# Kernel tuning notes

Measured on AMD Instinct MI355X. Metric: run time of the kernel, lower is better.

## Reference

```python
import jax, jax.numpy as jnp
import numpy as np

NS = 50000   # sentence (src) nodes, unit==1
NW = 50000   # word (dst) nodes, unit==0
E = 1600000  # sw edges
IN_DIM = 128
OUT_DIM = 64


def setup_inputs() -> dict:
    key = jax.random.key(0)
    k1, k2, k3, k4, k5, k6 = jax.random.split(key, 6)
    return {
        "h": jax.random.normal(k1, (NS, IN_DIM), dtype=jnp.float32),
        "W_fc": jax.random.normal(k2, (IN_DIM, OUT_DIM), dtype=jnp.float32) * 0.05,
        "w_attn": jax.random.normal(k3, (2 * OUT_DIM, 1), dtype=jnp.float32) * 0.05,
        "weight": jax.random.uniform(k4, (E,), dtype=jnp.float32),
        "src_idx": jax.random.randint(k5, (E,), 0, NS, dtype=jnp.int32),
        "dst_idx": jax.random.randint(k6, (E,), 0, NW, dtype=jnp.int32),
    }


def reference(h, W_fc, w_attn, weight, src_idx, dst_idx):
    # z = fc(h) on source (sentence) nodes only; dst (word) nodes have z == 0 in DGL
    z = h @ W_fc                                   # [NS, OUT_DIM]
    zs = z[src_idx]                                # [E, OUT_DIM] gather src features
    # attn_fc(cat(z_src, z_dst)) with z_dst == 0 -> only first half of w_attn acts
    wa_src = w_attn[:OUT_DIM, 0]                   # [OUT_DIM]
    e = jax.nn.leaky_relu(zs @ wa_src)             # [E], slope 0.01 (torch default)
    e = weight * e                                 # tfidf edge weight scaling
    # edge-softmax per destination node (segment softmax over ragged mailbox)
    m = jax.ops.segment_max(e, dst_idx, num_segments=NW)          # [NW]
    m = jnp.where(jnp.isfinite(m), m, 0.0)                        # empty nodes
    ex = jnp.exp(e - m[dst_idx])                                  # [E]
    den = jax.ops.segment_sum(ex, dst_idx, num_segments=NW)       # [NW]
    alpha = ex / jnp.where(den == 0.0, 1.0, den)[dst_idx]         # [E]
    # weighted scatter-sum of neighbor features into dst nodes
    out = jax.ops.segment_sum(alpha[:, None] * zs, dst_idx, num_segments=NW)
    return out                                     # [NW, OUT_DIM]
```

## Files before the change

kernel.cpp:

```cpp
#include <hip/hip_runtime.h>
#include <hip/hip_fp16.h>
#include <math.h>

#define NS_ 50000
#define NW_ 50000
#define IN_DIM_ 128
#define OUT_DIM_ 64

#define NSLAB 512
#define NB 1563
#define CAPS 1280
#define CAPP 2304

__device__ inline float leaky01(float x) { return x > 0.0f ? x : 0.01f * x; }

__global__ __launch_bounds__(256) void fc_kernel(const float* __restrict__ h,
                                                 const float* __restrict__ Wfc,
                                                 const float* __restrict__ w_attn,
                                                 __half* __restrict__ z16,
                                                 float* __restrict__ t) {
    __shared__ float hs[64 * IN_DIM_];
    int tid = threadIdx.x;
    int lane = tid & 63;
    int wv = tid >> 6;

    float Wc[IN_DIM_];
#pragma unroll
    for (int k = 0; k < IN_DIM_; ++k) Wc[k] = Wfc[k * OUT_DIM_ + lane];
    float wa = w_attn[lane];

    int row0 = blockIdx.x * 64;
    int nrows = NS_ - row0; if (nrows > 64) nrows = 64;

    const float4* hg = (const float4*)(h + (size_t)row0 * IN_DIM_);
    float4* hs4 = (float4*)hs;
    int nv = nrows * (IN_DIM_ / 4);
    for (int i = tid; i < nv; i += 256) hs4[i] = hg[i];
    __syncthreads();

    int rend = wv * 16 + 16; if (rend > nrows) rend = nrows;
    for (int r = wv * 16; r < rend; r += 2) {
        bool two = (r + 1 < rend);
        const float4* h0 = (const float4*)(hs + r * IN_DIM_);
        const float4* h1 = (const float4*)(hs + (two ? r + 1 : r) * IN_DIM_);
        float a0 = 0, a1 = 0, a2 = 0, a3 = 0;
        float b0 = 0, b1 = 0, b2 = 0, b3 = 0;
#pragma unroll
        for (int k4 = 0; k4 < IN_DIM_ / 4; ++k4) {
            float4 u = h0[k4];
            float4 v = h1[k4];
            a0 = fmaf(u.x, Wc[4 * k4 + 0], a0);
            a1 = fmaf(u.y, Wc[4 * k4 + 1], a1);
            a2 = fmaf(u.z, Wc[4 * k4 + 2], a2);
            a3 = fmaf(u.w, Wc[4 * k4 + 3], a3);
            b0 = fmaf(v.x, Wc[4 * k4 + 0], b0);
            b1 = fmaf(v.y, Wc[4 * k4 + 1], b1);
            b2 = fmaf(v.z, Wc[4 * k4 + 2], b2);
            b3 = fmaf(v.w, Wc[4 * k4 + 3], b3);
        }
        float za = (a0 + a1) + (a2 + a3);
        float zb = (b0 + b1) + (b2 + b3);
        z16[(size_t)(row0 + r) * OUT_DIM_ + lane] = __float2half(za);
        if (two) z16[(size_t)(row0 + r + 1) * OUT_DIM_ + lane] = __float2half(zb);
        float ta = za * wa, tb = zb * wa;
#pragma unroll
        for (int off = 32; off > 0; off >>= 1) {
            ta += __shfl_down(ta, off, 64);
            tb += __shfl_down(tb, off, 64);
        }
        if (lane == 0) {
            t[row0 + r] = ta;
            if (two) t[row0 + r + 1] = tb;
        }
    }
}

__global__ __launch_bounds__(1024) void partition_kernel(const float* __restrict__ weight,
                                                         const int* __restrict__ src,
                                                         const int* __restrict__ dst,
                                                         const float* __restrict__ t,
                                                         unsigned* __restrict__ meta_sb,
                                                         int2* __restrict__ edata,
                                                         int E, int slab_e) {
    __shared__ int hist[NB];
    __shared__ int cur[NB];
    __shared__ int wsum[16];
    int tid = threadIdx.x;
    int lane = tid & 63;
    int wv = tid >> 6;
    int s = blockIdx.x;
    int e0 = s * slab_e;
    int e1 = e0 + slab_e; if (e1 > E) e1 = E;
    int cnt = e1 - e0;

    for (int i = tid; i < NB; i += 1024) hist[i] = 0;
    __syncthreads();

    float exr0 = 0, exr1 = 0, exr2 = 0, exr3 = 0;
    int mr0 = 0, mr1 = 0, mr2 = 0, mr3 = 0;
#define PART_LOAD(P, EXR, MR)                                              \
    {                                                                      \
        int i = tid + (P) * 1024;                                          \
        if (i < cnt) {                                                     \
            int e = e0 + i;                                                \
            int sr = src[e];                                               \
            int d = dst[e];                                                \
            float ev = weight[e] * leaky01(t[sr]);                         \
            EXR = __expf(ev);                                              \
            MR = sr | ((d & 31) << 16) | ((d >> 5) << 21);                 \
            atomicAdd(&hist[d >> 5], 1);                                   \
        }                                                                  \
    }
    PART_LOAD(0, exr0, mr0)
    PART_LOAD(1, exr1, mr1)
    PART_LOAD(2, exr2, mr2)
    PART_LOAD(3, exr3, mr3)
#undef PART_LOAD
    __syncthreads();

    int i0 = 2 * tid, i1 = 2 * tid + 1;
    int h0 = (i0 < NB) ? hist[i0] : 0;
    int h1 = (i1 < NB) ? hist[i1] : 0;
    int pairv = h0 + h1;
    int incl = pairv;
#pragma unroll
    for (int off = 1; off < 64; off <<= 1) {
        int u = __shfl_up(incl, off, 64);
        if (lane >= off) incl += u;
    }
    if (lane == 63) wsum[wv] = incl;
    __syncthreads();
    int woff = 0;
    for (int w = 0; w < wv; ++w) woff += wsum[w];
    incl += woff;
    int base = incl - pairv;
    if (i0 < NB) {
        cur[i0] = base;
        meta_sb[(size_t)s * NB + i0] = ((unsigned)h0 << 16) | (unsigned)base;
    }
    if (i1 < NB) {
        int b1 = base + h0;
        cur[i1] = b1;
        meta_sb[(size_t)s * NB + i1] = ((unsigned)h1 << 16) | (unsigned)b1;
    }
    __syncthreads();

#define PART_STORE(P, EXR, MR)                                             \
    {                                                                      \
        int i = tid + (P) * 1024;                                          \
        if (i < cnt) {                                                     \
            int b = ((unsigned)MR) >> 21;                                  \
            int pos = atomicAdd(&cur[b], 1);                               \
            edata[e0 + pos] = make_int2(__float_as_int(EXR), MR & 0x1FFFFF); \
        }                                                                  \
    }
    PART_STORE(0, exr0, mr0)
    PART_STORE(1, exr1, mr1)
    PART_STORE(2, exr2, mr2)
    PART_STORE(3, exr3, mr3)
#undef PART_STORE
}

__global__ __launch_bounds__(256) void meta_transpose_kernel(const unsigned* __restrict__ meta,
                                                             unsigned* __restrict__ metaT) {
    __shared__ unsigned tile[64][65];
    int b0 = blockIdx.x * 64;
    int s0 = blockIdx.y * 64;
    int tx = threadIdx.x & 63, ty = threadIdx.x >> 6;
    for (int r = ty; r < 64; r += 4) {
        int b = b0 + tx;
        tile[r][tx] = (b < NB) ? meta[(size_t)(s0 + r) * NB + b] : 0u;
    }
    __syncthreads();
    for (int r = ty; r < 64; r += 4) {
        int b = b0 + r;
        if (b < NB) metaT[(size_t)b * NSLAB + s0 + tx] = tile[tx][r];
    }
}

__global__ __launch_bounds__(512) void aggregate_kernel(const unsigned* __restrict__ metaT,
                                                        const int2* __restrict__ edata,
                                                        const __half* __restrict__ z16,
                                                        float* __restrict__ out,
                                                        int slab_e) {
    __shared__ int2 sbuf[CAPS];
    __shared__ int2 sorted[CAPP];
    __shared__ unsigned short soff[NSLAB];
    __shared__ int arr[NSLAB + 1];
    __shared__ int wsum[8];
    __shared__ float dden[32];
    __shared__ int dcnt[32];
    __shared__ int dbase[33];

    int orig = blockIdx.x;
    {
        const int nwg = NB, nx = 8;
        int q = nwg / nx, r = nwg % nx;
        int xcd = orig % nx, idx = orig / nx;
        orig = (xcd < r) ? xcd * (q + 1) + idx : r * (q + 1) + (xcd - r) * q + idx;
    }
    int b = orig;
    int tid = threadIdx.x;
    int lane = tid & 63;
    int wv = tid >> 6;

    int cntv;
    {
        unsigned mv = metaT[(size_t)b * NSLAB + tid];
        soff[tid] = (unsigned short)(mv & 0xFFFFu);
        cntv = (int)(mv >> 16);
    }
    if (tid < 32) { dden[tid] = 0.0f; dcnt[tid] = 0; }
    for (int i = tid; i < CAPP; i += 512) sorted[i] = make_int2(0, 0);

    int incl = cntv;
#pragma unroll
    for (int off = 1; off < 64; off <<= 1) {
        int u = __shfl_up(incl, off, 64);
        if (lane >= off) incl += u;
    }
    if (lane == 63) wsum[wv] = incl;
    __syncthreads();
    int woff = 0;
    for (int w = 0; w < wv; ++w) woff += wsum[w];
    incl += woff;
    arr[tid + 1] = incl;
    if (tid == 0) arr[0] = 0;
    __syncthreads();

    int total = arr[NSLAB];
    if (total > CAPS) total = CAPS;

    int gid = tid >> 1, l2 = tid & 1;
    for (int s = gid; s < NSLAB; s += 256) {
        int base = arr[s];
        int len = arr[s + 1] - base;
        int so = (int)soff[s];
        for (int j = l2; j < len; j += 2) {
            int p = base + j;
            if (p < CAPS) {
                int2 e = edata[(size_t)s * slab_e + so + j];
                sbuf[p] = e;
                int d5 = (e.y >> 16) & 31;
                atomicAdd(&dcnt[d5], 1);
                atomicAdd(&dden[d5], __int_as_float(e.x));
            }
        }
    }
    __syncthreads();

    if (tid < 32) {
        int v = dcnt[tid];
        int pv = (v + 31) & ~31;
        int iv = pv;
#pragma unroll
        for (int off = 1; off < 32; off <<= 1) {
            int u = __shfl_up(iv, off, 64);
            if (tid >= off) iv += u;
        }
        dbase[tid + 1] = iv;
        dcnt[tid] = iv - pv;
        if (tid == 0) dbase[0] = 0;
    }
    __syncthreads();

    for (int k = tid; k < total; k += 512) {
        int2 e = sbuf[k];
        int d5 = (e.y >> 16) & 31;
        int pos = atomicAdd(&dcnt[d5], 1);
        if (pos < CAPP) sorted[pos] = e;
    }
    __syncthreads();

    int qg = lane >> 4;
    int dl = lane & 15;
    const unsigned short* z16u = (const unsigned short*)z16;
    for (int q = 0; q < 4; ++q) {
        int d5 = wv * 4 + q;
        int d = b * 32 + d5;
        if (d >= NW_) continue;
        int a0 = dbase[d5];
        int npad = dbase[d5 + 1] - a0;
        float dn = dden[d5];
        float invdn = (dn > 0.0f) ? 1.0f / dn : 0.0f;
        float c0 = 0.f, c1 = 0.f, c2 = 0.f, c3 = 0.f;
        for (int j = 0; j < npad; j += 32) {
            int2 ee[8];
#pragma unroll
            for (int u = 0; u < 8; ++u) ee[u] = sorted[a0 + j + u * 4 + qg];
            uint2 zz[8];
#pragma unroll
            for (int u = 0; u < 8; ++u) {
                int srcr = ee[u].y & 0xFFFF;
                zz[u] = *(const uint2*)(z16u + (size_t)srcr * 64 + dl * 4);
            }
#pragma unroll
            for (int u = 0; u < 8; ++u) {
                float ex = __int_as_float(ee[u].x);
                __half2 p0 = *(__half2*)&zz[u].x;
                __half2 p1 = *(__half2*)&zz[u].y;
                c0 = fmaf(ex, __low2float(p0), c0);
                c1 = fmaf(ex, __high2float(p0), c1);
                c2 = fmaf(ex, __low2float(p1), c2);
                c3 = fmaf(ex, __high2float(p1), c3);
            }
        }
        c0 += __shfl_xor(c0, 16, 64); c1 += __shfl_xor(c1, 16, 64);
        c2 += __shfl_xor(c2, 16, 64); c3 += __shfl_xor(c3, 16, 64);
        c0 += __shfl_xor(c0, 32, 64); c1 += __shfl_xor(c1, 32, 64);
        c2 += __shfl_xor(c2, 32, 64); c3 += __shfl_xor(c3, 32, 64);
        if (lane < 16) {
            float4 st = make_float4(c0 * invdn, c1 * invdn, c2 * invdn, c3 * invdn);
            *(float4*)(out + (size_t)d * OUT_DIM_ + lane * 4) = st;
        }
    }
}

extern "C" void kernel_launch(void* const* d_in, const int* in_sizes, int n_in,
                              void* d_out, int out_size, void* d_ws, size_t ws_size,
                              hipStream_t stream) {
    const float* h      = (const float*)d_in[0];
    const float* Wfc    = (const float*)d_in[1];
    const float* w_attn = (const float*)d_in[2];
    const float* weight = (const float*)d_in[3];
    const int*   src    = (const int*)d_in[4];
    const int*   dst    = (const int*)d_in[5];
    int E = in_sizes[3];
    float* out = (float*)d_out;

    int slab_e = (E + NSLAB - 1) / NSLAB;

    int2*     edata = (int2*)d_ws;
    __half*   z16   = (__half*)(edata + (size_t)E);
    float*    t     = (float*)(z16 + (size_t)NS_ * OUT_DIM_);
    unsigned* meta  = (unsigned*)(t + NS_);
    unsigned* metaT = meta + (size_t)NSLAB * NB;

    fc_kernel<<<(NS_ + 63) / 64, 256, 0, stream>>>(h, Wfc, w_attn, z16, t);

    partition_kernel<<<NSLAB, 1024, 0, stream>>>(weight, src, dst, t, meta, edata, E, slab_e);

    dim3 tg((NB + 63) / 64, NSLAB / 64);
    meta_transpose_kernel<<<tg, 256, 0, stream>>>(meta, metaT);

    aggregate_kernel<<<NB, 512, 0, stream>>>(metaT, edata, z16, out, slab_e);
}
```

Baseline: 101.8 us.

## Compute fc projection with fp16 MFMA and fold attention vector into W

Adds a one-block prep kernel that packs W_fc into fp16 MFMA B-fragment layout and precomputes W_fc·w_attn, so the attention score t comes straight from h in fp32. The fc kernel stages h as swizzled fp16 A-fragments in shared memory and uses 16x16x32 f16 MFMA instead of scalar FMA loops. The output goes through an LDS tile so z16 writes are coalesced. In exchange the matmul inputs are rounded to fp16, which reduces precision, and an extra small kernel launch is added.

```diff
diff --git a/kernel.cpp b/kernel.cpp
--- a/kernel.cpp
+++ b/kernel.cpp
@@ -12,65 +12,95 @@
 #define CAPS 1280
 #define CAPP 2304
 
+typedef _Float16 h16x8 __attribute__((ext_vector_type(8)));
+typedef float f32x4 __attribute__((ext_vector_type(4)));
+
 __device__ inline float leaky01(float x) { return x > 0.0f ? x : 0.01f * x; }
 
+__global__ __launch_bounds__(256) void prep_kernel(const float* __restrict__ Wfc,
+                                                   const float* __restrict__ w_attn,
+                                                   __half* __restrict__ W16f,
+                                                   float* __restrict__ wv128) {
+    int tid = threadIdx.x;
+    for (int i = tid; i < IN_DIM_ * OUT_DIM_; i += 256) {
+        int k = i >> 6, c = i & 63;
+        int ni = c >> 4, c16 = c & 15, kstep = k >> 5, ks = (k & 31) >> 3, el = k & 7;
+        W16f[(((ni * 4 + kstep) * 64) + ks * 16 + c16) * 8 + el] = __float2half(Wfc[i]);
+    }
+    if (tid < IN_DIM_) {
+        float s = 0.f;
+        for (int c = 0; c < OUT_DIM_; ++c) s += Wfc[tid * OUT_DIM_ + c] * w_attn[c];
+        wv128[tid] = s;
+    }
+}
+
 __global__ __launch_bounds__(256) void fc_kernel(const float* __restrict__ h,
-                                                 const float* __restrict__ Wfc,
-                                                 const float* __restrict__ w_attn,
+                                                 const __half* __restrict__ W16f,
+                                                 const float* __restrict__ wv128,
                                                  __half* __restrict__ z16,
                                                  float* __restrict__ t) {
-    __shared__ float hs[64 * IN_DIM_];
+    __shared__ __align__(16) __half Afrag[8192];
+    __shared__ float ztile[64][68];
     int tid = threadIdx.x;
     int lane = tid & 63;
     int wv = tid >> 6;
-
-    float Wc[IN_DIM_];
-#pragma unroll
-    for (int k = 0; k < IN_DIM_; ++k) Wc[k] = Wfc[k * OUT_DIM_ + lane];
-    float wa = w_attn[lane];
-
     int row0 = blockIdx.x * 64;
+
+    int k0 = (tid & 31) * 4;
+    float4 wvv = *(const float4*)(wv128 + k0);
+    int kstep = k0 >> 5, ks = (k0 & 31) >> 3, el = k0 & 7;
+#pragma unroll
+    for (int iter = 0; iter < 8; ++iter) {
+        int r = (tid >> 5) + iter * 8;
+        int row = row0 + r;
+        float4 hv = (row < NS_) ? *(const float4*)(h + (size_t)row * IN_DIM_ + k0)
+                                : make_float4(0.f, 0.f, 0.f, 0.f);
+        int slot = ((r >> 4) * 4 + kstep) * 64 + ks * 16 + (r & 15);
+        int slw = slot ^ ((slot >> 4) & 7);
+        __half2 lo = __floats2half2_rn(hv.x, hv.y);
+        __half2 hi = __floats2half2_rn(hv.z, hv.w);
+        uint2 pk = make_uint2(*(unsigned*)&lo, *(unsigned*)&hi);
+        *(uint2*)(&Afrag[slw * 8 + el]) = pk;
+        float pt = hv.x * wvv.x + hv.y * wvv.y + hv.z * wvv.z + hv.w * wvv.w;
+        pt += __shfl_down(pt, 16, 64);
+        pt += __shfl_down(pt, 8, 64);
+        pt += __shfl_down(pt, 4, 64);
+        pt += __shfl_down(pt, 2, 64);
+        pt += __shfl_down(pt, 1, 64);
+        if ((tid & 31) == 0 && row < NS_) t[row] = pt;
+    }
+    __syncthreads();
+
+    h16x8 af[4];
+#pragma unroll
+    for (int kst = 0; kst < 4; ++kst) {
+        int s = (wv * 4 + kst) * 64 + lane;
+        int sr = s ^ ((s >> 4) & 7);
+        af[kst] = *(const h16x8*)(&Afrag[sr * 8]);
+    }
+#pragma unroll
+    for (int ni = 0; ni < 4; ++ni) {
+        f32x4 acc = {0.f, 0.f, 0.f, 0.f};
+#pragma unroll
+        for (int kst = 0; kst < 4; ++kst) {
+            h16x8 bf = *(const h16x8*)(W16f + ((size_t)(ni * 4 + kst) * 64 + lane) * 8);
+            acc = __builtin_amdgcn_mfma_f32_16x16x32_f16(af[kst], bf, acc, 0, 0, 0);
+        }
+        int col = ni * 16 + (lane & 15);
+        int rb = wv * 16 + (lane >> 4) * 4;
+        ztile[rb + 0][col] = acc[0];
+        ztile[rb + 1][col] = acc[1];
+        ztile[rb + 2][col] = acc[2];
+        ztile[rb + 3][col] = acc[3];
+    }
+    __syncthreads();
+
     int nrows = NS_ - row0; if (nrows > 64) nrows = 64;
-
-    const float4* hg = (const float4*)(h + (size_t)row0 * IN_DIM_);
-    float4* hs4 = (float4*)hs;
-    int nv = nrows * (IN_DIM_ / 4);
-    for (int i = tid; i < nv; i += 256) hs4[i] = hg[i];
-    __syncthreads();
-
-    int rend = wv * 16 + 16; if (rend > nrows) rend = nrows;
-    for (int r = wv * 16; r < rend; r += 2) {
-        bool two = (r + 1 < rend);
-        const float4* h0 = (const float4*)(hs + r * IN_DIM_);
-        const float4* h1 = (const float4*)(hs + (two ? r + 1 : r) * IN_DIM_);
-        float a0 = 0, a1 = 0, a2 = 0, a3 = 0;
-        float b0 = 0, b1 = 0, b2 = 0, b3 = 0;
-#pragma unroll
-        for (int k4 = 0; k4 < IN_DIM_ / 4; ++k4) {
-            float4 u = h0[k4];
-            float4 v = h1[k4];
-            a0 = fmaf(u.x, Wc[4 * k4 + 0], a0);
-            a1 = fmaf(u.y, Wc[4 * k4 + 1], a1);
-            a2 = fmaf(u.z, Wc[4 * k4 + 2], a2);
-            a3 = fmaf(u.w, Wc[4 * k4 + 3], a3);
-            b0 = fmaf(v.x, Wc[4 * k4 + 0], b0);
-            b1 = fmaf(v.y, Wc[4 * k4 + 1], b1);
-            b2 = fmaf(v.z, Wc[4 * k4 + 2], b2);
-            b3 = fmaf(v.w, Wc[4 * k4 + 3], b3);
-        }
-        float za = (a0 + a1) + (a2 + a3);
-        float zb = (b0 + b1) + (b2 + b3);
-        z16[(size_t)(row0 + r) * OUT_DIM_ + lane] = __float2half(za);
-        if (two) z16[(size_t)(row0 + r + 1) * OUT_DIM_ + lane] = __float2half(zb);
-        float ta = za * wa, tb = zb * wa;
-#pragma unroll
-        for (int off = 32; off > 0; off >>= 1) {
-            ta += __shfl_down(ta, off, 64);
-            tb += __shfl_down(tb, off, 64);
-        }
-        if (lane == 0) {
-            t[row0 + r] = ta;
-            if (two) t[row0 + r + 1] = tb;
+    for (int j = tid; j < 64 * 32; j += 256) {
+        int r = j >> 5, c0 = (j & 31) * 2;
+        if (r < nrows) {
+            __half2 hp = __floats2half2_rn(ztile[r][c0], ztile[r][c0 + 1]);
+            *(__half2*)(z16 + (size_t)(row0 + r) * OUT_DIM_ + c0) = hp;
         }
     }
 }
@@ -335,8 +365,12 @@
     float*    t     = (float*)(z16 + (size_t)NS_ * OUT_DIM_);
     unsigned* meta  = (unsigned*)(t + NS_);
     unsigned* metaT = meta + (size_t)NSLAB * NB;
-
-    fc_kernel<<<(NS_ + 63) / 64, 256, 0, stream>>>(h, Wfc, w_attn, z16, t);
+    __half*   W16f  = (__half*)(metaT + (size_t)NSLAB * NB);
+    float*    wv128 = (float*)(W16f + 8192);
+
+    prep_kernel<<<1, 256, 0, stream>>>(Wfc, w_attn, W16f, wv128);
+
+    fc_kernel<<<(NS_ + 63) / 64, 256, 0, stream>>>(h, W16f, wv128, z16, t);
 
     partition_kernel<<<NSLAB, 1024, 0, stream>>>(weight, src, dst, t, meta, edata, E, slab_e);
 
```

Result: faster. 85.24 us (-16.2%).
